# Kernel tuning notes

Hardware: AMD Instinct MI355X
Metric: run time of the kernel (lower is better)

Reference implementation:

```python
import jax, jax.numpy as jnp
import numpy as np

VOCAB, EMBED, HIDDEN, PAD = 32000, 512, 1024, 3

def setup_inputs() -> dict:
    key = jax.random.key(0)
    ks = jax.random.split(key, 7)
    B, S = 16, 256
    input_ids = jax.random.randint(ks[0], (B, S), 0, VOCAB)
    hidden = jnp.zeros((B, HIDDEN), dtype=jnp.float32)
    sc = 0.02
    emb_table = jax.random.normal(ks[1], (VOCAB, EMBED), jnp.float32) * sc
    Wxh_w = jax.random.normal(ks[2], (HIDDEN, EMBED), jnp.float32) * sc
    Wxh_b = jax.random.normal(ks[3], (HIDDEN,), jnp.float32) * sc
    Whh_w = jax.random.normal(ks[4], (HIDDEN, HIDDEN), jnp.float32) * sc
    Who_w = jax.random.normal(ks[5], (VOCAB, HIDDEN), jnp.float32) * sc
    Who_b = jax.random.normal(ks[6], (VOCAB,), jnp.float32) * sc
    return {"input_ids": input_ids, "hidden": hidden, "emb_table": emb_table,
            "Wxh_w": Wxh_w, "Wxh_b": Wxh_b, "Whh_w": Whh_w,
            "Who_w": Who_w, "Who_b": Who_b}

def reference(input_ids, hidden, emb_table, Wxh_w, Wxh_b, Whh_w, Who_w, Who_b):
    # padding_idx: row PAD of the embedding is zero
    pad_mask = (jnp.arange(VOCAB) != PAD).astype(emb_table.dtype)
    table = emb_table * pad_mask[:, None]
    embeds = table[input_ids]                      # [B, S, E]
    # precompute input projection for all steps: [B, S, H]
    xproj = jnp.einsum('bse,he->bsh', embeds, Wxh_w) + Wxh_b

    def step(h, xp_t):                             # xp_t: [B, H]
        h_new = jnp.tanh(xp_t + h @ Whh_w.T)
        return h_new, h_new

    h_final, h_all = jax.lax.scan(step, hidden, jnp.swapaxes(xproj, 0, 1))
    # h_all: [S, B, H] -> logits [B, S, V]
    logits = jnp.einsum('sbh,vh->bsv', h_all, Who_w) + Who_b
    return (logits, h_final)
```

## Files before the change

### kernel.cpp

```cpp
#include <hip/hip_runtime.h>
#include <stdint.h>

#define NB 16
#define NS 256
#define NV 32000
#define NE 512
#define NH 1024
#define PAD_IDX 3

#define WS_XP    0L
#define WS_HCH   16777216L
#define WS_WHO   25198592L
#define WS_FLG   90734592L
#define WS_NEED  90800384L

typedef __attribute__((ext_vector_type(8))) short bf16x8;
typedef __attribute__((ext_vector_type(4))) float f32x4;
typedef __attribute__((ext_vector_type(4))) uint32_t u32x4;

__device__ __forceinline__ uint16_t f2bf(float f){
  union { float f; uint32_t u; } v; v.f = f;
  return (uint16_t)((v.u + 0x7fffu + ((v.u >> 16) & 1u)) >> 16);
}

__device__ __forceinline__ bf16x8 pack8(float4 a, float4 b){
  bf16x8 r;
  r[0]=(short)f2bf(a.x); r[1]=(short)f2bf(a.y); r[2]=(short)f2bf(a.z); r[3]=(short)f2bf(a.w);
  r[4]=(short)f2bf(b.x); r[5]=(short)f2bf(b.y); r[6]=(short)f2bf(b.z); r[7]=(short)f2bf(b.w);
  return r;
}

__device__ __forceinline__ u32x4 load_coh16(const void* p){
  u32x4 r;
  asm volatile("global_load_dwordx4 %0, %1, off sc0 sc1" : "=v"(r) : "v"(p) : "memory");
  return r;
}
__device__ __forceinline__ uint32_t load_coh4(const void* p){
  uint32_t r;
  asm volatile("global_load_dword %0, %1, off sc0 sc1" : "=v"(r) : "v"(p) : "memory");
  return r;
}
__device__ __forceinline__ void store_coh8(void* p, uint64_t v){
  asm volatile("global_store_dwordx2 %0, %1, off sc0 sc1" :: "v"(p), "v"(v) : "memory");
}
__device__ __forceinline__ void store_coh4(void* p, uint32_t v){
  asm volatile("global_store_dword %0, %1, off sc0 sc1" :: "v"(p), "v"(v) : "memory");
}
__device__ __forceinline__ void store_nt4(void* p, float v){
  asm volatile("global_store_dword %0, %1, off nt" :: "v"(p), "v"(v) : "memory");
}

__device__ __forceinline__ u32x4 umax4(u32x4 a, u32x4 b){
  u32x4 r;
  r[0] = a[0] > b[0] ? a[0] : b[0];
  r[1] = a[1] > b[1] ? a[1] : b[1];
  r[2] = a[2] > b[2] ? a[2] : b[2];
  r[3] = a[3] > b[3] ? a[3] : b[3];
  return r;
}

__device__ __forceinline__ float tanh_fast(float x){
  x = fminf(fmaxf(x, -10.f), 10.f);
  float t = __builtin_amdgcn_exp2f(x * 2.885390081777927f);
  return (t - 1.0f) * __builtin_amdgcn_rcpf(t + 1.0f);
}

__global__ void k_init(const float* __restrict__ hidden, uint16_t* __restrict__ hch,
                       uint32_t* __restrict__ flg){
  long idx = (long)blockIdx.x * 256 + threadIdx.x;
  ((u32x4*)(hch + (long)NB * NH))[idx] = (u32x4){~0u, ~0u, ~0u, ~0u};
  if (idx < NB * NH) hch[idx] = f2bf(hidden[idx]);
  if (idx < 512) flg[idx] = 0u;
}

__global__ void k_cvt(const float* __restrict__ src, uint32_t* __restrict__ dst){
  long idx = (long)blockIdx.x * 256 + threadIdx.x;
  const float4* p = (const float4*)src;
  float4 a = p[idx*2], b = p[idx*2+1];
  u32x4 d;
  d[0] = (uint32_t)f2bf(a.x) | ((uint32_t)f2bf(a.y) << 16);
  d[1] = (uint32_t)f2bf(a.z) | ((uint32_t)f2bf(a.w) << 16);
  d[2] = (uint32_t)f2bf(b.x) | ((uint32_t)f2bf(b.y) << 16);
  d[3] = (uint32_t)f2bf(b.z) | ((uint32_t)f2bf(b.w) << 16);
  ((u32x4*)dst)[idx] = d;
}

__global__ __launch_bounds__(256) void k_xproj(
    const int* __restrict__ ids, const float* __restrict__ tab,
    const float* __restrict__ wxh, const float* __restrict__ bxh,
    float* __restrict__ xp){
  int bid = blockIdx.x;
  int tm = bid & 63, tn = bid >> 6;
  int Mb = tm * 64, Nb = tn * 64;
  int tid = threadIdx.x;
  int w = tid >> 6, l = tid & 63;
  int lr = l & 15, lk = l >> 4;

  int m = Mb + w*16 + lr;
  int id = ids[m];
  const float* arow = tab + (long)id * NE;
  bool pad = (id == PAD_IDX);

  f32x4 acc[4];
  #pragma unroll
  for (int j = 0; j < 4; ++j) acc[j] = (f32x4){0.f,0.f,0.f,0.f};

  for (int k0 = 0; k0 < NE; k0 += 32){
    int k = k0 + lk*8;
    bf16x8 af = (bf16x8){0,0,0,0,0,0,0,0};
    if (!pad){
      float4 a = *(const float4*)(arow + k);
      float4 b = *(const float4*)(arow + k + 4);
      af = pack8(a, b);
    }
    #pragma unroll
    for (int j = 0; j < 4; ++j){
      const float* brow = wxh + (long)(Nb + j*16 + lr) * NE + k;
      float4 x = *(const float4*)brow;
      float4 y = *(const float4*)(brow + 4);
      bf16x8 bf_ = pack8(x, y);
      acc[j] = __builtin_amdgcn_mfma_f32_16x16x32_bf16(af, bf_, acc[j], 0, 0, 0);
    }
  }
  #pragma unroll
  for (int j = 0; j < 4; ++j){
    int n = Nb + j*16 + lr;
    float bias = bxh[n];
    #pragma unroll
    for (int r = 0; r < 4; ++r){
      int row = Mb + w*16 + lk*4 + r;
      xp[(long)row * NH + n] = acc[j][r] + bias;
    }
  }
}

__global__ __launch_bounds__(256, 2) void k_fused(
    const float* __restrict__ whh, const float* __restrict__ xp,
    uint16_t* __restrict__ hch, const uint16_t* __restrict__ whobf,
    const float* __restrict__ whob, uint32_t* __restrict__ allvis,
    uint32_t* __restrict__ fin, float* __restrict__ out,
    float* __restrict__ hfin){
  __shared__ __align__(16) char smem[17*1024];
  const int bid = blockIdx.x;
  const int tid = threadIdx.x;

  if (bid < 64){
    if (tid >= 128) return;
    float*    accbuf = (float*)smem;
    uint16_t* hs2    = (uint16_t*)(smem + 2048);
    const int wv = tid >> 6;
    const int l  = tid & 63;
    const int j0 = bid * 16;
    const int lr = l & 15, lk = l >> 4;
    __builtin_amdgcn_s_setprio(2);

    bf16x8 bfrag[16];
    #pragma unroll
    for (int kk = 0; kk < 16; ++kk){
      const float* s0 = whh + (long)(j0 + lr) * NH + (wv*16 + kk)*32 + lk*8;
      float4 a = *(const float4*)s0;
      float4 b = *(const float4*)(s0 + 4);
      bfrag[kk] = pack8(a, b);
    }

    float xpreg[4];
    if (wv == 0){
      #pragma unroll
      for (int r = 0; r < 4; ++r)
        xpreg[r] = xp[((long)(lk*4 + r) * NS + 0) * NH + j0 + lr];
    }

    const char* hbase = (const char*)hch;
    for (int t = 0; t < NS; ++t){
      const char* hsrc = hbase + (long)t * NB * NH * 2 + lr * 2048 + wv * 1024 + lk * 16;
      u32x4 hfrag[16];
      while (true){
        #pragma unroll
        for (int kk = 0; kk < 16; ++kk)
          hfrag[kk] = load_coh16(hsrc + kk * 64);
        asm volatile("s_waitcnt vmcnt(0)" ::: "memory");
        __builtin_amdgcn_sched_barrier(0);
        u32x4 m4 = hfrag[0];
        #pragma unroll
        for (int kk = 1; kk < 16; ++kk) m4 = umax4(m4, hfrag[kk]);
        uint32_t m01 = m4[0] > m4[1] ? m4[0] : m4[1];
        uint32_t m23 = m4[2] > m4[3] ? m4[2] : m4[3];
        uint32_t m = m01 > m23 ? m01 : m23;
        if (__all(m != 0xFFFFFFFFu)) break;
      }
      __builtin_amdgcn_sched_barrier(0);

      f32x4 a0 = (f32x4){0.f,0.f,0.f,0.f}, a1 = a0, a2 = a0, a3 = a0;
      #pragma unroll
      for (int kk = 0; kk < 16; kk += 4){
        a0 = __builtin_amdgcn_mfma_f32_16x16x32_bf16(*(const bf16x8*)&hfrag[kk  ], bfrag[kk  ], a0, 0, 0, 0);
        a1 = __builtin_amdgcn_mfma_f32_16x16x32_bf16(*(const bf16x8*)&hfrag[kk+1], bfrag[kk+1], a1, 0, 0, 0);
        a2 = __builtin_amdgcn_mfma_f32_16x16x32_bf16(*(const bf16x8*)&hfrag[kk+2], bfrag[kk+2], a2, 0, 0, 0);
        a3 = __builtin_amdgcn_mfma_f32_16x16x32_bf16(*(const bf16x8*)&hfrag[kk+3], bfrag[kk+3], a3, 0, 0, 0);
      }
      f32x4 acc = (a0 + a1) + (a2 + a3);

      if (wv == 1)
        *(f32x4*)&accbuf[((t & 1)*64 + l)*4] = acc;
      __syncthreads();

      if (wv == 0){
        if (bid == 0 && l == 0) store_coh4(allvis + t, 1u);
        f32x4 o = *(const f32x4*)&accbuf[((t & 1)*64 + l)*4];
        uint16_t* hb = hs2 + (t & 1)*256;
        #pragma unroll
        for (int r = 0; r < 4; ++r){
          int b = lk*4 + r;
          float hv = tanh_fast(xpreg[r] + acc[r] + o[r]);
          hb[b*16 + lr] = f2bf(hv);
          if (t == NS-1) hfin[b*NH + j0 + lr] = hv;
        }
        asm volatile("s_waitcnt lgkmcnt(0)" ::: "memory");
        __builtin_amdgcn_sched_barrier(0);
        int rb = l >> 2, cc = l & 3;
        uint32_t w0 = *(const uint32_t*)&hb[rb*16 + cc*4];
        uint32_t w1 = *(const uint32_t*)&hb[rb*16 + cc*4 + 2];
        char* dst = (char*)hch + (long)(t+1) * NB * NH * 2 + rb * 2048 + j0*2 + cc*8;
        store_coh8(dst, ((uint64_t)w1 << 32) | (uint64_t)w0);
        if (t + 1 < NS){
          #pragma unroll
          for (int r = 0; r < 4; ++r)
            xpreg[r] = xp[((long)(lk*4 + r) * NS + (t+1)) * NH + j0 + lr];
        }
      }
    }
    if (wv == 0){
      asm volatile("s_waitcnt vmcnt(0)" ::: "memory");
      if (l == 0) store_coh4(fin + bid, 1u);
    }
    return;
  }

  uint16_t* As = (uint16_t*)smem;
  uint16_t* Bs = (uint16_t*)(smem + 8192);
  int tile = bid - 64;
  int tm = tile / 250;
  int tn = tile % 250;
  int Mb = tm * 128, Nb = tn * 128;
  int hs = tm * 8 + 8;

  if (hs < 256){
    while (true){
      uint32_t f = load_coh4(allvis + hs);
      asm volatile("s_waitcnt vmcnt(0)" ::: "memory");
      __builtin_amdgcn_sched_barrier(0);
      if (__syncthreads_count(f == 0u) == 0) break;
      __builtin_amdgcn_s_sleep(16);
    }
  } else {
    const uint32_t* gp = fin + (tid & 63);
    while (true){
      uint32_t f = load_coh4(gp);
      asm volatile("s_waitcnt vmcnt(0)" ::: "memory");
      __builtin_amdgcn_sched_barrier(0);
      if (__syncthreads_count(f == 0u) == 0) break;
      __builtin_amdgcn_s_sleep(16);
    }
  }

  int wv = tid >> 6, l = tid & 63;
  int wm = wv >> 1, wn = wv & 1;
  int lr = l & 15, lk = l >> 4;

  int r0 = tid >> 2, c0 = tid & 3;
  int r1 = r0 + 64;
  const uint16_t* pa0 = hch + (long)(Mb + r0 + 16) * NH + c0*8;
  const uint16_t* pa1 = hch + (long)(Mb + r1 + 16) * NH + c0*8;
  const uint16_t* pb0 = whobf + (long)(Nb + r0) * NH + c0*8;
  const uint16_t* pb1 = whobf + (long)(Nb + r1) * NH + c0*8;
  int da0 = r0*4 + (c0 ^ (r0 & 3));
  int da1 = r1*4 + (c0 ^ (r1 & 3));

  u32x4 ra0 = *(const u32x4*)pa0;
  u32x4 ra1 = *(const u32x4*)pa1;
  u32x4 rb0 = *(const u32x4*)pb0;
  u32x4 rb1 = *(const u32x4*)pb1;

  f32x4 acc[4][4];
  #pragma unroll
  for (int i = 0; i < 4; ++i)
    #pragma unroll
    for (int jj = 0; jj < 4; ++jj) acc[i][jj] = (f32x4){0.f,0.f,0.f,0.f};

  for (int kt = 0; kt < 32; ++kt){
    ((u32x4*)As)[da0] = ra0;
    ((u32x4*)As)[da1] = ra1;
    ((u32x4*)Bs)[da0] = rb0;
    ((u32x4*)Bs)[da1] = rb1;
    __syncthreads();
    if (kt != 31){
      int off = (kt + 1) * 32;
      ra0 = *(const u32x4*)(pa0 + off);
      ra1 = *(const u32x4*)(pa1 + off);
      rb0 = *(const u32x4*)(pb0 + off);
      rb1 = *(const u32x4*)(pb1 + off);
    }
    bf16x8 af[4], bg_[4];
    #pragma unroll
    for (int i = 0; i < 4; ++i){
      int ra = wm*64 + i*16 + lr;
      int rb = wn*64 + i*16 + lr;
      af[i]  = *(const bf16x8*)&((const u32x4*)As)[ra*4 + (lk ^ (ra & 3))];
      bg_[i] = *(const bf16x8*)&((const u32x4*)Bs)[rb*4 + (lk ^ (rb & 3))];
    }
    #pragma unroll
    for (int i = 0; i < 4; ++i)
      #pragma unroll
      for (int jj = 0; jj < 4; ++jj)
        acc[i][jj] = __builtin_amdgcn_mfma_f32_16x16x32_bf16(af[i], bg_[jj], acc[i][jj], 0, 0, 0);
    __syncthreads();
  }

  #pragma unroll
  for (int jj = 0; jj < 4; ++jj){
    int col = Nb + wn*64 + jj*16 + lr;
    float bias = whob[col];
    #pragma unroll
    for (int i = 0; i < 4; ++i){
      #pragma unroll
      for (int rr = 0; rr < 4; ++rr){
        int m = Mb + wm*64 + i*16 + lk*4 + rr;
        long orow = (long)((m & 15) * 256 + (m >> 4));
        store_nt4(&out[orow * NV + col], acc[i][jj][rr] + bias);
      }
    }
  }
}

extern "C" void kernel_launch(void* const* d_in, const int* in_sizes, int n_in,
                              void* d_out, int out_size, void* d_ws, size_t ws_size,
                              hipStream_t stream){
  (void)in_sizes; (void)n_in; (void)out_size;
  if (ws_size < (size_t)WS_NEED) return;

  const int*   ids    = (const int*)  d_in[0];
  const float* hidden = (const float*)d_in[1];
  const float* table  = (const float*)d_in[2];
  const float* wxh    = (const float*)d_in[3];
  const float* bxh    = (const float*)d_in[4];
  const float* whh    = (const float*)d_in[5];
  const float* who    = (const float*)d_in[6];
  const float* whob   = (const float*)d_in[7];

  char* ws = (char*)d_ws;
  float*    xp     = (float*)   (ws + WS_XP);
  uint16_t* hchain = (uint16_t*)(ws + WS_HCH);
  uint16_t* whobf  = (uint16_t*)(ws + WS_WHO);
  uint32_t* allvis = (uint32_t*)(ws + WS_FLG);
  uint32_t* fin    = allvis + 260;
  float* out    = (float*)d_out;
  float* hfinal = out + (long)NB * NS * NV;

  k_init <<<2048,  256, 0, stream>>>(hidden, hchain, allvis);
  k_cvt  <<<16000, 256, 0, stream>>>(who, (uint32_t*)whobf);
  k_xproj<<<1024,  256, 0, stream>>>(ids, table, wxh, bxh, xp);
  k_fused<<<8064,  256, 0, stream>>>(whh, xp, hchain, whobf, whob,
                                     allvis, fin, out, hfinal);
}
```

Baseline: 1.157 ms.

## Merge prep kernels and make logits GEMM a persistent atomic tile scheduler

```diff
diff --git a/kernel.cpp b/kernel.cpp
--- a/kernel.cpp
+++ b/kernel.cpp
@@ -47,7 +47,7 @@
   asm volatile("global_store_dword %0, %1, off sc0 sc1" :: "v"(p), "v"(v) : "memory");
 }
 __device__ __forceinline__ void store_nt4(void* p, float v){
-  asm volatile("global_store_dword %0, %1, off nt" :: "v"(p), "v"(v) : "memory");
+  asm volatile("global_store_dword %0, %1, off sc1 nt" :: "v"(p), "v"(v) : "memory");
 }
 
 __device__ __forceinline__ u32x4 umax4(u32x4 a, u32x4 b){
@@ -65,71 +65,76 @@
   return (t - 1.0f) * __builtin_amdgcn_rcpf(t + 1.0f);
 }
 
-__global__ void k_init(const float* __restrict__ hidden, uint16_t* __restrict__ hch,
-                       uint32_t* __restrict__ flg){
-  long idx = (long)blockIdx.x * 256 + threadIdx.x;
-  ((u32x4*)(hch + (long)NB * NH))[idx] = (u32x4){~0u, ~0u, ~0u, ~0u};
-  if (idx < NB * NH) hch[idx] = f2bf(hidden[idx]);
-  if (idx < 512) flg[idx] = 0u;
-}
-
-__global__ void k_cvt(const float* __restrict__ src, uint32_t* __restrict__ dst){
-  long idx = (long)blockIdx.x * 256 + threadIdx.x;
-  const float4* p = (const float4*)src;
-  float4 a = p[idx*2], b = p[idx*2+1];
-  u32x4 d;
-  d[0] = (uint32_t)f2bf(a.x) | ((uint32_t)f2bf(a.y) << 16);
-  d[1] = (uint32_t)f2bf(a.z) | ((uint32_t)f2bf(a.w) << 16);
-  d[2] = (uint32_t)f2bf(b.x) | ((uint32_t)f2bf(b.y) << 16);
-  d[3] = (uint32_t)f2bf(b.z) | ((uint32_t)f2bf(b.w) << 16);
-  ((u32x4*)dst)[idx] = d;
-}
-
-__global__ __launch_bounds__(256) void k_xproj(
-    const int* __restrict__ ids, const float* __restrict__ tab,
-    const float* __restrict__ wxh, const float* __restrict__ bxh,
-    float* __restrict__ xp){
+__global__ __launch_bounds__(256) void k_pre(
+    const float* __restrict__ hidden, uint16_t* __restrict__ hch,
+    uint32_t* __restrict__ flg, const float* __restrict__ who,
+    uint32_t* __restrict__ whodst, const int* __restrict__ ids,
+    const float* __restrict__ tab, const float* __restrict__ wxh,
+    const float* __restrict__ bxh, float* __restrict__ xp){
   int bid = blockIdx.x;
-  int tm = bid & 63, tn = bid >> 6;
-  int Mb = tm * 64, Nb = tn * 64;
   int tid = threadIdx.x;
-  int w = tid >> 6, l = tid & 63;
-  int lr = l & 15, lk = l >> 4;
-
-  int m = Mb + w*16 + lr;
-  int id = ids[m];
-  const float* arow = tab + (long)id * NE;
-  bool pad = (id == PAD_IDX);
-
-  f32x4 acc[4];
-  #pragma unroll
-  for (int j = 0; j < 4; ++j) acc[j] = (f32x4){0.f,0.f,0.f,0.f};
-
-  for (int k0 = 0; k0 < NE; k0 += 32){
-    int k = k0 + lk*8;
-    bf16x8 af = (bf16x8){0,0,0,0,0,0,0,0};
-    if (!pad){
-      float4 a = *(const float4*)(arow + k);
-      float4 b = *(const float4*)(arow + k + 4);
-      af = pack8(a, b);
+
+  if (bid < 2048){
+    long idx = (long)bid * 256 + tid;
+    ((u32x4*)(hch + (long)NB * NH))[idx] = (u32x4){~0u, ~0u, ~0u, ~0u};
+    if (idx < NB * NH) hch[idx] = f2bf(hidden[idx]);
+    if (idx < 512) flg[idx] = 0u;
+    return;
+  }
+  if (bid < 18048){
+    long idx = (long)(bid - 2048) * 256 + tid;
+    const float4* p = (const float4*)who;
+    float4 a = p[idx*2], b = p[idx*2+1];
+    u32x4 d;
+    d[0] = (uint32_t)f2bf(a.x) | ((uint32_t)f2bf(a.y) << 16);
+    d[1] = (uint32_t)f2bf(a.z) | ((uint32_t)f2bf(a.w) << 16);
+    d[2] = (uint32_t)f2bf(b.x) | ((uint32_t)f2bf(b.y) << 16);
+    d[3] = (uint32_t)f2bf(b.z) | ((uint32_t)f2bf(b.w) << 16);
+    ((u32x4*)whodst)[idx] = d;
+    return;
+  }
+  {
+    int xb = bid - 18048;
+    int tm = xb & 63, tn = xb >> 6;
+    int Mb = tm * 64, Nb = tn * 64;
+    int w = tid >> 6, l = tid & 63;
+    int lr = l & 15, lk = l >> 4;
+
+    int m = Mb + w*16 + lr;
+    int id = ids[m];
+    const float* arow = tab + (long)id * NE;
+    bool pad = (id == PAD_IDX);
+
+    f32x4 acc[4];
+    #pragma unroll
+    for (int j = 0; j < 4; ++j) acc[j] = (f32x4){0.f,0.f,0.f,0.f};
+
+    for (int k0 = 0; k0 < NE; k0 += 32){
+      int k = k0 + lk*8;
+      bf16x8 af = (bf16x8){0,0,0,0,0,0,0,0};
+      if (!pad){
+        float4 a = *(const float4*)(arow + k);
+        float4 b = *(const float4*)(arow + k + 4);
+        af = pack8(a, b);
+      }
+      #pragma unroll
+      for (int j = 0; j < 4; ++j){
+        const float* brow = wxh + (long)(Nb + j*16 + lr) * NE + k;
+        float4 x = *(const float4*)brow;
+        float4 y = *(const float4*)(brow + 4);
+        bf16x8 bf_ = pack8(x, y);
+        acc[j] = __builtin_amdgcn_mfma_f32_16x16x32_bf16(af, bf_, acc[j], 0, 0, 0);
+      }
     }
     #pragma unroll
     for (int j = 0; j < 4; ++j){
-      const float* brow = wxh + (long)(Nb + j*16 + lr) * NE + k;
-      float4 x = *(const float4*)brow;
-      float4 y = *(const float4*)(brow + 4);
-      bf16x8 bf_ = pack8(x, y);
-      acc[j] = __builtin_amdgcn_mfma_f32_16x16x32_bf16(af, bf_, acc[j], 0, 0, 0);
-    }
-  }
-  #pragma unroll
-  for (int j = 0; j < 4; ++j){
-    int n = Nb + j*16 + lr;
-    float bias = bxh[n];
-    #pragma unroll
-    for (int r = 0; r < 4; ++r){
-      int row = Mb + w*16 + lk*4 + r;
-      xp[(long)row * NH + n] = acc[j][r] + bias;
+      int n = Nb + j*16 + lr;
+      float bias = bxh[n];
+      #pragma unroll
+      for (int r = 0; r < 4; ++r){
+        int row = Mb + w*16 + lk*4 + r;
+        xp[(long)row * NH + n] = acc[j][r] + bias;
+      }
     }
   }
 }
@@ -138,9 +143,10 @@
     const float* __restrict__ whh, const float* __restrict__ xp,
     uint16_t* __restrict__ hch, const uint16_t* __restrict__ whobf,
     const float* __restrict__ whob, uint32_t* __restrict__ allvis,
-    uint32_t* __restrict__ fin, float* __restrict__ out,
-    float* __restrict__ hfin){
+    uint32_t* __restrict__ fin, uint32_t* __restrict__ cnt,
+    float* __restrict__ out, float* __restrict__ hfin){
   __shared__ __align__(16) char smem[17*1024];
+  __shared__ int tsh;
   const int bid = blockIdx.x;
   const int tid = threadIdx.x;
 
@@ -238,95 +244,102 @@
 
   uint16_t* As = (uint16_t*)smem;
   uint16_t* Bs = (uint16_t*)(smem + 8192);
-  int tile = bid - 64;
-  int tm = tile / 250;
-  int tn = tile % 250;
-  int Mb = tm * 128, Nb = tn * 128;
-  int hs = tm * 8 + 8;
-
-  if (hs < 256){
-    while (true){
-      uint32_t f = load_coh4(allvis + hs);
-      asm volatile("s_waitcnt vmcnt(0)" ::: "memory");
-      __builtin_amdgcn_sched_barrier(0);
-      if (__syncthreads_count(f == 0u) == 0) break;
-      __builtin_amdgcn_s_sleep(16);
-    }
-  } else {
-    const uint32_t* gp = fin + (tid & 63);
-    while (true){
-      uint32_t f = load_coh4(gp);
-      asm volatile("s_waitcnt vmcnt(0)" ::: "memory");
-      __builtin_amdgcn_sched_barrier(0);
-      if (__syncthreads_count(f == 0u) == 0) break;
-      __builtin_amdgcn_s_sleep(16);
-    }
-  }
-
   int wv = tid >> 6, l = tid & 63;
   int wm = wv >> 1, wn = wv & 1;
   int lr = l & 15, lk = l >> 4;
-
   int r0 = tid >> 2, c0 = tid & 3;
   int r1 = r0 + 64;
-  const uint16_t* pa0 = hch + (long)(Mb + r0 + 16) * NH + c0*8;
-  const uint16_t* pa1 = hch + (long)(Mb + r1 + 16) * NH + c0*8;
-  const uint16_t* pb0 = whobf + (long)(Nb + r0) * NH + c0*8;
-  const uint16_t* pb1 = whobf + (long)(Nb + r1) * NH + c0*8;
   int da0 = r0*4 + (c0 ^ (r0 & 3));
   int da1 = r1*4 + (c0 ^ (r1 & 3));
 
-  u32x4 ra0 = *(const u32x4*)pa0;
-  u32x4 ra1 = *(const u32x4*)pa1;
-  u32x4 rb0 = *(const u32x4*)pb0;
-  u32x4 rb1 = *(const u32x4*)pb1;
-
-  f32x4 acc[4][4];
-  #pragma unroll
-  for (int i = 0; i < 4; ++i)
-    #pragma unroll
-    for (int jj = 0; jj < 4; ++jj) acc[i][jj] = (f32x4){0.f,0.f,0.f,0.f};
-
-  for (int kt = 0; kt < 32; ++kt){
-    ((u32x4*)As)[da0] = ra0;
-    ((u32x4*)As)[da1] = ra1;
-    ((u32x4*)Bs)[da0] = rb0;
-    ((u32x4*)Bs)[da1] = rb1;
+  while (true){
+    if (tid == 0)
+      tsh = (int)__hip_atomic_fetch_add(cnt, 1u, __ATOMIC_RELAXED, __HIP_MEMORY_SCOPE_AGENT);
     __syncthreads();
-    if (kt != 31){
-      int off = (kt + 1) * 32;
-      ra0 = *(const u32x4*)(pa0 + off);
-      ra1 = *(const u32x4*)(pa1 + off);
-      rb0 = *(const u32x4*)(pb0 + off);
-      rb1 = *(const u32x4*)(pb1 + off);
-    }
-    bf16x8 af[4], bg_[4];
-    #pragma unroll
-    for (int i = 0; i < 4; ++i){
-      int ra = wm*64 + i*16 + lr;
-      int rb = wn*64 + i*16 + lr;
-      af[i]  = *(const bf16x8*)&((const u32x4*)As)[ra*4 + (lk ^ (ra & 3))];
-      bg_[i] = *(const bf16x8*)&((const u32x4*)Bs)[rb*4 + (lk ^ (rb & 3))];
-    }
+    int tile = tsh;
+    if (tile >= 8000) break;
+
+    int tm = tile / 250;
+    int tn = tile % 250;
+    int Mb = tm * 128, Nb = tn * 128;
+    int hs = tm * 8 + 8;
+
+    if (hs < 256){
+      while (true){
+        uint32_t f = load_coh4(allvis + hs);
+        asm volatile("s_waitcnt vmcnt(0)" ::: "memory");
+        __builtin_amdgcn_sched_barrier(0);
+        if (__syncthreads_count(f == 0u) == 0) break;
+        __builtin_amdgcn_s_sleep(16);
+      }
+    } else {
+      const uint32_t* gp = fin + (tid & 63);
+      while (true){
+        uint32_t f = load_coh4(gp);
+        asm volatile("s_waitcnt vmcnt(0)" ::: "memory");
+        __builtin_amdgcn_sched_barrier(0);
+        if (__syncthreads_count(f == 0u) == 0) break;
+        __builtin_amdgcn_s_sleep(16);
+      }
+    }
+
+    const uint16_t* pa0 = hch + (long)(Mb + r0 + 16) * NH + c0*8;
+    const uint16_t* pa1 = hch + (long)(Mb + r1 + 16) * NH + c0*8;
+    const uint16_t* pb0 = whobf + (long)(Nb + r0) * NH + c0*8;
+    const uint16_t* pb1 = whobf + (long)(Nb + r1) * NH + c0*8;
+
+    u32x4 ra0 = *(const u32x4*)pa0;
+    u32x4 ra1 = *(const u32x4*)pa1;
+    u32x4 rb0 = *(const u32x4*)pb0;
+    u32x4 rb1 = *(const u32x4*)pb1;
+
+    f32x4 acc[4][4];
     #pragma unroll
     for (int i = 0; i < 4; ++i)
       #pragma unroll
-      for (int jj = 0; jj < 4; ++jj)
-        acc[i][jj] = __builtin_amdgcn_mfma_f32_16x16x32_bf16(af[i], bg_[jj], acc[i][jj], 0, 0, 0);
-    __syncthreads();
-  }
-
-  #pragma unroll
-  for (int jj = 0; jj < 4; ++jj){
-    int col = Nb + wn*64 + jj*16 + lr;
-    float bias = whob[col];
-    #pragma unroll
-    for (int i = 0; i < 4; ++i){
-      #pragma unroll
-      for (int rr = 0; rr < 4; ++rr){
-        int m = Mb + wm*64 + i*16 + lk*4 + rr;
-        long orow = (long)((m & 15) * 256 + (m >> 4));
-        store_nt4(&out[orow * NV + col], acc[i][jj][rr] + bias);
+      for (int jj = 0; jj < 4; ++jj) acc[i][jj] = (f32x4){0.f,0.f,0.f,0.f};
+
+    for (int kt = 0; kt < 32; ++kt){
+      ((u32x4*)As)[da0] = ra0;
+      ((u32x4*)As)[da1] = ra1;
+      ((u32x4*)Bs)[da0] = rb0;
+      ((u32x4*)Bs)[da1] = rb1;
+      __syncthreads();
+      if (kt != 31){
+        int off = (kt + 1) * 32;
+        ra0 = *(const u32x4*)(pa0 + off);
+        ra1 = *(const u32x4*)(pa1 + off);
+        rb0 = *(const u32x4*)(pb0 + off);
+        rb1 = *(const u32x4*)(pb1 + off);
+      }
+      bf16x8 af[4], bg_[4];
+      #pragma unroll
+      for (int i = 0; i < 4; ++i){
+        int ra = wm*64 + i*16 + lr;
+        int rb = wn*64 + i*16 + lr;
+        af[i]  = *(const bf16x8*)&((const u32x4*)As)[ra*4 + (lk ^ (ra & 3))];
+        bg_[i] = *(const bf16x8*)&((const u32x4*)Bs)[rb*4 + (lk ^ (rb & 3))];
+      }
+      #pragma unroll
+      for (int i = 0; i < 4; ++i)
+        #pragma unroll
+        for (int jj = 0; jj < 4; ++jj)
+          acc[i][jj] = __builtin_amdgcn_mfma_f32_16x16x32_bf16(af[i], bg_[jj], acc[i][jj], 0, 0, 0);
+      __syncthreads();
+    }
+
+    #pragma unroll
+    for (int jj = 0; jj < 4; ++jj){
+      int col = Nb + wn*64 + jj*16 + lr;
+      float bias = whob[col];
+      #pragma unroll
+      for (int i = 0; i < 4; ++i){
+        #pragma unroll
+        for (int rr = 0; rr < 4; ++rr){
+          int m = Mb + wm*64 + i*16 + lk*4 + rr;
+          long orow = (long)((m & 15) * 256 + (m >> 4));
+          store_nt4(&out[orow * NV + col], acc[i][jj][rr] + bias);
+        }
       }
     }
   }
@@ -353,12 +366,12 @@
   uint16_t* whobf  = (uint16_t*)(ws + WS_WHO);
   uint32_t* allvis = (uint32_t*)(ws + WS_FLG);
   uint32_t* fin    = allvis + 260;
+  uint32_t* cnt    = allvis + 324;
   float* out    = (float*)d_out;
   float* hfinal = out + (long)NB * NS * NV;
 
-  k_init <<<2048,  256, 0, stream>>>(hidden, hchain, allvis);
-  k_cvt  <<<16000, 256, 0, stream>>>(who, (uint32_t*)whobf);
-  k_xproj<<<1024,  256, 0, stream>>>(ids, table, wxh, bxh, xp);
-  k_fused<<<8064,  256, 0, stream>>>(whh, xp, hchain, whobf, whob,
-                                     allvis, fin, out, hfinal);
-}
+  k_pre  <<<19072, 256, 0, stream>>>(hidden, hchain, allvis, who,
+                                     (uint32_t*)whobf, ids, table, wxh, bxh, xp);
+  k_fused<<<448,   256, 0, stream>>>(whh, xp, hchain, whobf, whob,
+                                     allvis, fin, cnt, out, hfinal);
+}
```

New measurement: 1.212 ms. +4.7%, slower.
